# Kernel optimization log

Measured on AMD Instinct MI355X. Metric: run time of the kernel, lower is better.

The kernel has to match this reference:

```python
import jax, jax.numpy as jnp
import numpy as np

B, S, D, H = 2, 2048, 2048, 16
DH = D // H
EPS = 1e-5


def layernorm(x, gamma, beta):
    mu = jnp.mean(x, axis=-1, keepdims=True)
    var = jnp.var(x, axis=-1, keepdims=True)
    return (x - mu) * jax.lax.rsqrt(var + EPS) * gamma + beta


def setup_inputs() -> dict:
    key = jax.random.key(0)
    ks = jax.random.split(key, 10)
    sc = 1.0 / np.sqrt(D)
    return {
        "x": jax.random.normal(ks[0], (B, S, D), dtype=jnp.float32),
        "wq": jax.random.normal(ks[1], (D, D), dtype=jnp.float32) * sc,
        "bq": jnp.zeros((D,), jnp.float32),
        "wk": jax.random.normal(ks[2], (D, D), dtype=jnp.float32) * sc,
        "bk": jnp.zeros((D,), jnp.float32),
        "wv": jax.random.normal(ks[3], (D, D), dtype=jnp.float32) * sc,
        "bv": jnp.zeros((D,), jnp.float32),
        "wf": jax.random.normal(ks[4], (D, D), dtype=jnp.float32) * sc,
        "bf": jnp.zeros((D,), jnp.float32),
        "gamma": jnp.ones((D,), jnp.float32),
        "beta": jnp.zeros((D,), jnp.float32),
    }


def reference(x, wq, bq, wk, bk, wv, bv, wf, bf, gamma, beta):
    q = x @ wq + bq
    k = x @ wk + bk
    v = x @ wv + bv
    # split: [B,S,D] -> [B,H,S,DH]
    split = lambda t: t.reshape(B, S, H, DH).transpose(0, 2, 1, 3)
    q, k, v = split(q), split(k), split(v)
    s = jnp.einsum("bhqd,bhkd->bhqk", q, k) / np.sqrt(DH)
    p = jax.nn.softmax(s, axis=-1)
    o = jnp.einsum("bhqk,bhkd->bhqd", p, v)
    # faithful to original buggy concat: flat view of [B,H,S,DH] as [B,S,H*DH]
    o = o.reshape(B, S, H * DH)
    vb = o
    h1 = layernorm(o + x, gamma, beta)
    h2 = h1 @ wf + bf
    out = layernorm(h2 + vb, gamma, beta)
    return out
```

## Files before the change

### kernel.cpp

```cpp
#include <hip/hip_runtime.h>


#define B_ 2
#define S_ 2048
#define D_ 2048
#define H_ 16
#define DH_ 128

typedef __attribute__((ext_vector_type(8))) short s16x8;
typedef __attribute__((ext_vector_type(8))) unsigned short u16x8;
typedef __attribute__((ext_vector_type(4))) float f32x4;
typedef __attribute__((ext_vector_type(4))) unsigned short u16x4;

#define MFMA16(a, b, c) __builtin_amdgcn_mfma_f32_16x16x32_bf16(a, b, c, 0, 0, 0)

__device__ inline unsigned short f2bf(float f) {
  union { float f; unsigned u; } x; x.f = f;
  unsigned r = (x.u + 0x7fffu + ((x.u >> 16) & 1u)) >> 16;
  return (unsigned short)r;
}
__device__ inline float bf2f(unsigned short u) {
  union { unsigned u; float f; } x; x.u = ((unsigned)u) << 16;
  return x.f;
}
__device__ inline unsigned pack2bf(float a, float b) {
  unsigned ua = __builtin_bit_cast(unsigned, a) + 0x8000u;
  unsigned ub = __builtin_bit_cast(unsigned, b) + 0x8000u;
  return __builtin_amdgcn_perm(ub, ua, 0x07060302u);
}

__device__ inline void gld_lds16(const void* g, void* l) {
  __builtin_amdgcn_global_load_lds(
      (__attribute__((address_space(1))) void*)g,
      (__attribute__((address_space(3))) void*)l, 16, 0, 0);
}

__global__ __launch_bounds__(256) void prep_kernel(
    const float* __restrict__ x, unsigned short* __restrict__ xb,
    const float* __restrict__ w0, const float* __restrict__ w1,
    const float* __restrict__ w2, const float* __restrict__ w3,
    unsigned short* __restrict__ o0, unsigned short* __restrict__ o1,
    unsigned short* __restrict__ o2, unsigned short* __restrict__ o3) {
  int z = blockIdx.z;
  int t = threadIdx.x;
  if (z == 4) {
    int base = (blockIdx.y * 32 + blockIdx.x) * 16384 + t * 4;
#pragma unroll
    for (int p = 0; p < 16; ++p) {
      int i = base + p * 1024;
      float4 v = *(const float4*)&x[i];
      u16x4 o;
      o.x = f2bf(v.x); o.y = f2bf(v.y); o.z = f2bf(v.z); o.w = f2bf(v.w);
      *(u16x4*)&xb[i] = o;
    }
    return;
  }
  const float* W = z == 0 ? w0 : z == 1 ? w1 : z == 2 ? w2 : w3;
  unsigned short* WT = z == 0 ? o0 : z == 1 ? o1 : z == 2 ? o2 : o3;
  int n0 = blockIdx.x * 64, k0 = blockIdx.y * 128;
  int cl = t & 15, rw = t >> 4;
  int kb = k0 + rw * 8, nb = n0 + cl * 4;
  float4 f[8];
#pragma unroll
  for (int r = 0; r < 8; ++r) f[r] = *(const float4*)&W[(kb + r) * D_ + nb];
#define TPOSE(comp, i)                                                      \
  {                                                                         \
    u16x8 o = {f2bf(f[0].comp), f2bf(f[1].comp), f2bf(f[2].comp),           \
               f2bf(f[3].comp), f2bf(f[4].comp), f2bf(f[5].comp),           \
               f2bf(f[6].comp), f2bf(f[7].comp)};                           \
    *(u16x8*)&WT[(nb + i) * D_ + kb] = o;                                   \
  }
  TPOSE(x, 0) TPOSE(y, 1) TPOSE(z, 2) TPOSE(w, 3)
#undef TPOSE
}

__global__ __launch_bounds__(256) void gemm_qkv_kernel(
    const unsigned short* __restrict__ A, const unsigned short* __restrict__ W0,
    const unsigned short* __restrict__ W1, const unsigned short* __restrict__ W2,
    const float* __restrict__ b0, const float* __restrict__ b1,
    const float* __restrict__ b2, unsigned short* __restrict__ Qb,
    unsigned short* __restrict__ Kb, unsigned short* __restrict__ Vt,
    float qscale) {
  __shared__ short As[128 * 64];
  __shared__ short Bs[128 * 64];
  int wi = blockIdx.x >> 4;
  int n0 = (blockIdx.x & 15) * 128;
  const unsigned short* BT = wi == 0 ? W0 : wi == 1 ? W1 : W2;
  const float* bias = wi == 0 ? b0 : wi == 1 ? b1 : b2;
  float oscale = wi == 0 ? qscale : 1.0f;

  int t = threadIdx.x, lane = t & 63, w = t >> 6;
  int nl = lane & 15, q = lane >> 4;
  int m0 = blockIdx.y * 128;
  int wr = (w >> 1) * 64, wc = (w & 1) * 64;
  int swz = nl & 7;

  f32x4 acc[4][4];
  f32x4 z4 = {0.f, 0.f, 0.f, 0.f};
#pragma unroll
  for (int i = 0; i < 4; ++i)
#pragma unroll
    for (int j = 0; j < 4; ++j) acc[i][j] = z4;

  for (int kk = 0; kk < 2048; kk += 64) {
    __syncthreads();
#pragma unroll
    for (int i2 = 0; i2 < 4; ++i2) {
      int c = t + 256 * i2;
      int row = c >> 3, dc = (c & 7) ^ (row & 7);
      gld_lds16(&A[(m0 + row) * 2048 + kk + dc * 8], &As[c * 8]);
      gld_lds16(&BT[(n0 + row) * 2048 + kk + dc * 8], &Bs[c * 8]);
    }
    __syncthreads();
#pragma unroll
    for (int kc = 0; kc < 2; ++kc) {
      s16x8 af[4], bf[4];
#pragma unroll
      for (int i = 0; i < 4; ++i)
        af[i] = *(const s16x8*)&As[(wr + i * 16 + nl) * 64 +
                                   (((kc << 2) + q) ^ swz) * 8];
#pragma unroll
      for (int j = 0; j < 4; ++j)
        bf[j] = *(const s16x8*)&Bs[(wc + j * 16 + nl) * 64 +
                                   (((kc << 2) + q) ^ swz) * 8];
#pragma unroll
      for (int i = 0; i < 4; ++i)
#pragma unroll
        for (int j = 0; j < 4; ++j) acc[i][j] = MFMA16(af[i], bf[j], acc[i][j]);
    }
  }
#pragma unroll
  for (int i = 0; i < 4; ++i)
#pragma unroll
    for (int j = 0; j < 4; ++j) {
      int row = m0 + wr + i * 16 + q * 4;
      int col = n0 + wc + j * 16 + nl;
      float bv = bias[col];
      float v[4];
#pragma unroll
      for (int r = 0; r < 4; ++r) v[r] = (acc[i][j][r] + bv) * oscale;
      if (wi == 2) {
        unsigned d0 = pack2bf(v[0], v[1]), d1 = pack2bf(v[2], v[3]);
        long idx = ((long)(((row >> 11) * 16 + (col >> 7)) * 128 + (col & 127))) * 2048 +
                   (row & 2047);
        *(uint2*)&Vt[idx] = (uint2){d0, d1};
      } else {
        unsigned short* out = wi == 0 ? Qb : Kb;
#pragma unroll
        for (int r = 0; r < 4; ++r)
          out[(row + r) * 2048 + col] = f2bf(v[r]);
      }
    }
}

__global__ __launch_bounds__(256) void gemm_ff_kernel(
    const unsigned short* __restrict__ A, const unsigned short* __restrict__ BT,
    const float* __restrict__ bias, unsigned short* __restrict__ Cout) {
  __shared__ short As[128 * 64];
  __shared__ short Bs[128 * 64];
  int t = threadIdx.x, lane = t & 63, w = t >> 6;
  int nl = lane & 15, q = lane >> 4;
  int m0 = blockIdx.y * 128, n0 = blockIdx.x * 128;
  int wr = (w >> 1) * 64, wc = (w & 1) * 64;
  int swz = nl & 7;

  f32x4 acc[4][4];
  f32x4 z4 = {0.f, 0.f, 0.f, 0.f};
#pragma unroll
  for (int i = 0; i < 4; ++i)
#pragma unroll
    for (int j = 0; j < 4; ++j) acc[i][j] = z4;

  for (int kk = 0; kk < 2048; kk += 64) {
    __syncthreads();
#pragma unroll
    for (int i2 = 0; i2 < 4; ++i2) {
      int c = t + 256 * i2;
      int row = c >> 3, dc = (c & 7) ^ (row & 7);
      gld_lds16(&A[(m0 + row) * 2048 + kk + dc * 8], &As[c * 8]);
      gld_lds16(&BT[(n0 + row) * 2048 + kk + dc * 8], &Bs[c * 8]);
    }
    __syncthreads();
#pragma unroll
    for (int kc = 0; kc < 2; ++kc) {
      s16x8 af[4], bf[4];
#pragma unroll
      for (int i = 0; i < 4; ++i)
        af[i] = *(const s16x8*)&As[(wr + i * 16 + nl) * 64 +
                                   (((kc << 2) + q) ^ swz) * 8];
#pragma unroll
      for (int j = 0; j < 4; ++j)
        bf[j] = *(const s16x8*)&Bs[(wc + j * 16 + nl) * 64 +
                                   (((kc << 2) + q) ^ swz) * 8];
#pragma unroll
      for (int i = 0; i < 4; ++i)
#pragma unroll
        for (int j = 0; j < 4; ++j) acc[i][j] = MFMA16(af[i], bf[j], acc[i][j]);
    }
  }
#pragma unroll
  for (int i = 0; i < 4; ++i)
#pragma unroll
    for (int j = 0; j < 4; ++j) {
      int row = m0 + wr + i * 16 + q * 4;
      int col = n0 + wc + j * 16 + nl;
      float bv = bias[col];
#pragma unroll
      for (int r = 0; r < 4; ++r)
        Cout[(row + r) * 2048 + col] = f2bf(acc[i][j][r] + bv);
    }
}

__global__ __launch_bounds__(256, 2) void attn_kernel(
    const unsigned short* __restrict__ Q, const unsigned short* __restrict__ K,
    const unsigned short* __restrict__ VT, unsigned short* __restrict__ O) {
  __shared__ short KsA[8192], KsB[8192];
  __shared__ short VsA[8192], VsB[8192];
  __shared__ short Ps[8192];
  int t = threadIdx.x, lane = t & 63, w = t >> 6;
  int nl = lane & 15, q = lane >> 4;
  int i = blockIdx.x;
  int qb = i >> 5;
  int bh = (i & 7) + 8 * ((i >> 3) & 3);
  int b = bh >> 4, h = bh & 15;

  s16x8 qf[2][4];
  int qrow = b * S_ + qb * 128 + w * 32;
#pragma unroll
  for (int t2 = 0; t2 < 2; ++t2)
#pragma unroll
    for (int kc = 0; kc < 4; ++kc)
      qf[t2][kc] = *(const s16x8*)&Q[(qrow + t2 * 16 + nl) * D_ + h * DH_ + kc * 32 + q * 8];

  f32x4 z4 = {0.f, 0.f, 0.f, 0.f};
  f32x4 accO[2][8];
  f32x4 l4[2] = {z4, z4};
#pragma unroll
  for (int t2 = 0; t2 < 2; ++t2)
#pragma unroll
    for (int n8 = 0; n8 < 8; ++n8) accO[t2][n8] = z4;

  int swz = nl & 7;

  const unsigned short* kp[4];
  const unsigned short* vp[4];
#pragma unroll
  for (int i2 = 0; i2 < 4; ++i2) {
    int c = t + 256 * i2;
    int s = c >> 4, p = c & 15;
    kp[i2] = K + (long)(b * S_ + s) * D_ + h * DH_ + ((p ^ (s & 7)) * 8);
    int d = c >> 3, cp = c & 7, cs = cp ^ (d & 7);
    vp[i2] = VT + (long)(bh * DH_ + d) * S_ + cs * 8;
  }

#define STAGE(bufK, bufV)                           \
  {                                                 \
    _Pragma("unroll") for (int i2 = 0; i2 < 4; ++i2) { \
      gld_lds16(kp[i2], &bufK[(t + 256 * i2) * 8]); \
      gld_lds16(vp[i2], &bufV[(t + 256 * i2) * 8]); \
      kp[i2] += 64 * D_;                            \
      vp[i2] += 64;                                 \
    }                                               \
  }

  auto compute = [&](const short* Ks, const short* Vs) {
    f32x4 accS[2][4];
#pragma unroll
    for (int t2 = 0; t2 < 2; ++t2)
#pragma unroll
      for (int n = 0; n < 4; ++n) accS[t2][n] = z4;
    __builtin_amdgcn_s_setprio(1);
#pragma unroll
    for (int kc = 0; kc < 4; ++kc) {
      s16x8 kf[4];
#pragma unroll
      for (int n = 0; n < 4; ++n)
        kf[n] = *(const s16x8*)&Ks[(n * 16 + nl) * 128 +
                                   ((((kc << 2) + q) ^ swz)) * 8];
#pragma unroll
      for (int t2 = 0; t2 < 2; ++t2)
#pragma unroll
        for (int n = 0; n < 4; ++n)
          accS[t2][n] = MFMA16(kf[n], qf[t2][kc], accS[t2][n]);
    }
    __builtin_amdgcn_s_setprio(0);

#pragma unroll
    for (int t2 = 0; t2 < 2; ++t2) {
      int prow = (w * 32 + t2 * 16 + nl) * 64;
#pragma unroll
      for (int n = 0; n < 4; ++n) {
#pragma unroll
        for (int r = 0; r < 4; ++r)
          accS[t2][n][r] = __builtin_amdgcn_exp2f(accS[t2][n][r] - 16.0f);
        l4[t2] += accS[t2][n];
        unsigned d0 = pack2bf(accS[t2][n][0], accS[t2][n][1]);
        unsigned d1 = pack2bf(accS[t2][n][2], accS[t2][n][3]);
        int c8 = q + 4 * n;
        int off = prow + (((c8 >> 1) ^ swz) * 8 + (c8 & 1) * 4);
        *(uint2*)&Ps[off] = (uint2){d0, d1};
      }
    }

    __builtin_amdgcn_s_setprio(1);
#pragma unroll
    for (int ks = 0; ks < 2; ++ks) {
      s16x8 pf[2];
#pragma unroll
      for (int t2 = 0; t2 < 2; ++t2)
        pf[t2] = *(const s16x8*)&Ps[(w * 32 + t2 * 16 + nl) * 64 + ((4 * ks + q) ^ swz) * 8];
#pragma unroll
      for (int n8 = 0; n8 < 8; ++n8) {
        int d = n8 * 16 + nl;
        int cs = ks * 4 + q;
        int ci = d * 8 + (cs ^ (d & 7));
        s16x8 vf = *(const s16x8*)&Vs[ci * 8];
#pragma unroll
        for (int t2 = 0; t2 < 2; ++t2)
          accO[t2][n8] = MFMA16(vf, pf[t2], accO[t2][n8]);
      }
    }
    __builtin_amdgcn_s_setprio(0);
  };

  STAGE(KsA, VsA);
  for (int it = 0; it < 32; it += 2) {
    __syncthreads();
    STAGE(KsB, VsB);
    compute(KsA, VsA);
    __syncthreads();
    if (it + 2 < 32) STAGE(KsA, VsA);
    compute(KsB, VsB);
  }
#undef STAGE

#pragma unroll
  for (int t2 = 0; t2 < 2; ++t2) {
    float l = (l4[t2][0] + l4[t2][1]) + (l4[t2][2] + l4[t2][3]);
    l += __shfl_xor(l, 16);
    l += __shfl_xor(l, 32);
    float inv = 1.0f / l;
    int s = qb * 128 + w * 32 + t2 * 16 + nl;
    unsigned short* orow = &O[((long)(bh * S_ + s)) * DH_];
#pragma unroll
    for (int n8 = 0; n8 < 8; ++n8) {
      unsigned d0 = pack2bf(accO[t2][n8][0] * inv, accO[t2][n8][1] * inv);
      unsigned d1 = pack2bf(accO[t2][n8][2] * inv, accO[t2][n8][3] * inv);
      *(uint2*)&orow[n8 * 16 + q * 4] = (uint2){d0, d1};
    }
  }
}

template <int OUTBF, int INBF>
__global__ __launch_bounds__(256) void ln_kernel(
    const void* __restrict__ Ain, const unsigned short* __restrict__ Ob,
    const float* __restrict__ gamma, const float* __restrict__ beta,
    void* __restrict__ out) {
  int row = blockIdx.x, t = threadIdx.x;
  int lane = t & 63, w = t >> 6;
  int c0 = t * 8;
  float v[8], s = 0.f, s2 = 0.f;
  u16x8 ob = *(const u16x8*)&Ob[row * D_ + c0];
  if (INBF) {
    u16x8 a = *(const u16x8*)&((const unsigned short*)Ain)[row * D_ + c0];
#pragma unroll
    for (int p = 0; p < 8; ++p) v[p] = bf2f(a[p]);
  } else {
    float4 a0 = *(const float4*)&((const float*)Ain)[row * D_ + c0];
    float4 a1 = *(const float4*)&((const float*)Ain)[row * D_ + c0 + 4];
    v[0] = a0.x; v[1] = a0.y; v[2] = a0.z; v[3] = a0.w;
    v[4] = a1.x; v[5] = a1.y; v[6] = a1.z; v[7] = a1.w;
  }
#pragma unroll
  for (int p = 0; p < 8; ++p) {
    v[p] += bf2f(ob[p]);
    s += v[p]; s2 += v[p] * v[p];
  }
#pragma unroll
  for (int mk = 32; mk >= 1; mk >>= 1) {
    s += __shfl_xor(s, mk);
    s2 += __shfl_xor(s2, mk);
  }
  __shared__ float red[8];
  if (lane == 0) { red[w * 2] = s; red[w * 2 + 1] = s2; }
  __syncthreads();
  s = red[0] + red[2] + red[4] + red[6];
  s2 = red[1] + red[3] + red[5] + red[7];
  float mu = s * (1.0f / D_);
  float var = s2 * (1.0f / D_) - mu * mu;
  float rs = rsqrtf(var + 1e-5f);
  float4 g0 = *(const float4*)&gamma[c0], g1 = *(const float4*)&gamma[c0 + 4];
  float4 b0 = *(const float4*)&beta[c0], b1 = *(const float4*)&beta[c0 + 4];
  float g[8] = {g0.x, g0.y, g0.z, g0.w, g1.x, g1.y, g1.z, g1.w};
  float bb[8] = {b0.x, b0.y, b0.z, b0.w, b1.x, b1.y, b1.z, b1.w};
  float o[8];
#pragma unroll
  for (int p = 0; p < 8; ++p) o[p] = (v[p] - mu) * rs * g[p] + bb[p];
  if (OUTBF) {
    u16x8 ov;
#pragma unroll
    for (int p = 0; p < 8; ++p) ov[p] = f2bf(o[p]);
    *(u16x8*)&((unsigned short*)out)[row * D_ + c0] = ov;
  } else {
    float4 o0 = {o[0], o[1], o[2], o[3]}, o1 = {o[4], o[5], o[6], o[7]};
    *(float4*)&((float*)out)[row * D_ + c0] = o0;
    *(float4*)&((float*)out)[row * D_ + c0 + 4] = o1;
  }
}

extern "C" void kernel_launch(void* const* d_in, const int* in_sizes, int n_in,
                              void* d_out, int out_size, void* d_ws, size_t ws_size,
                              hipStream_t stream) {
  const float* x     = (const float*)d_in[0];
  const float* wq    = (const float*)d_in[1];
  const float* bq    = (const float*)d_in[2];
  const float* wk    = (const float*)d_in[3];
  const float* bk    = (const float*)d_in[4];
  const float* wv    = (const float*)d_in[5];
  const float* bv    = (const float*)d_in[6];
  const float* wf    = (const float*)d_in[7];
  const float* bfb   = (const float*)d_in[8];
  const float* gamma = (const float*)d_in[9];
  const float* beta  = (const float*)d_in[10];

  unsigned short* ws  = (unsigned short*)d_ws;
  unsigned short* WqT = ws;
  unsigned short* WkT = ws + 4194304;
  unsigned short* WvT = ws + 8388608;
  unsigned short* WfT = ws + 12582912;
  unsigned short* Xb  = ws + 16777216;
  unsigned short* Qb  = ws + 25165824;
  unsigned short* Kb  = ws + 33554432;
  unsigned short* Vt  = ws + 41943040;
  unsigned short* Ob  = Xb;
  unsigned short* H1  = Kb;
  unsigned short* H2b = Vt;

  const float scl2 = 0.08838834764831845f * 1.4426950408889634f;

  dim3 blk(256);
  prep_kernel<<<dim3(32, 16, 5), blk, 0, stream>>>(
      x, Xb, wq, wk, wv, wf, WqT, WkT, WvT, WfT);

  gemm_qkv_kernel<<<dim3(48, 32), blk, 0, stream>>>(
      Xb, WqT, WkT, WvT, bq, bk, bv, Qb, Kb, Vt, scl2);

  attn_kernel<<<dim3(512), blk, 0, stream>>>(Qb, Kb, Vt, Ob);

  ln_kernel<1, 0><<<dim3(4096), blk, 0, stream>>>(x, Ob, gamma, beta, (void*)H1);
  gemm_ff_kernel<<<dim3(16, 32), blk, 0, stream>>>(H1, WfT, bfb, H2b);
  ln_kernel<0, 1><<<dim3(4096), blk, 0, stream>>>(H2b, Ob, gamma, beta, d_out);
}
```

Measured before the change: 404.0 us.

## Replace GEMM kernels with 8-wave 256x128 triple-buffered pipelined GEMM

Merges the QKV and FF GEMMs into one templated kernel that uses 512 threads and a 256x128 output tile. A three-stage LDS ring prefetches K-tiles two iterations ahead, replacing the old load-then-sync-then-compute loop. The kernel also raises MFMA priority with s_setprio and remaps block IDs across XCDs, all to hide global-load latency and improve L2 locality. In exchange it uses far more LDS (144 KB) and allows only one block per CU, so latency hiding depends on the hand-written waitcnt schedule.

```diff
diff --git a/kernel.cpp b/kernel.cpp
--- a/kernel.cpp
+++ b/kernel.cpp
@@ -74,27 +74,54 @@
 #undef TPOSE
 }
 
-__global__ __launch_bounds__(256) void gemm_qkv_kernel(
+template <int QKV>
+__global__ __launch_bounds__(512, 1) void gemm8p_kernel(
     const unsigned short* __restrict__ A, const unsigned short* __restrict__ W0,
     const unsigned short* __restrict__ W1, const unsigned short* __restrict__ W2,
     const float* __restrict__ b0, const float* __restrict__ b1,
     const float* __restrict__ b2, unsigned short* __restrict__ Qb,
     unsigned short* __restrict__ Kb, unsigned short* __restrict__ Vt,
     float qscale) {
-  __shared__ short As[128 * 64];
-  __shared__ short Bs[128 * 64];
-  int wi = blockIdx.x >> 4;
-  int n0 = (blockIdx.x & 15) * 128;
-  const unsigned short* BT = wi == 0 ? W0 : wi == 1 ? W1 : W2;
-  const float* bias = wi == 0 ? b0 : wi == 1 ? b1 : b2;
-  float oscale = wi == 0 ? qscale : 1.0f;
+  __shared__ short As3[3][256 * 64];
+  __shared__ short Bs3[3][128 * 64];
+  int idx = blockIdx.x;
+  const int nwg = QKV ? 768 : 256;
+  const int cpx = nwg >> 3;
+  int wg = (idx & 7) * cpx + (idx >> 3);
+  int wi, mt, ntile;
+  if (QKV) {
+    wi = wg >> 8;
+    int rem = wg & 255;
+    mt = rem >> 4; ntile = rem & 15;
+  } else {
+    wi = 0; mt = wg >> 4; ntile = wg & 15;
+  }
+  int m0 = mt * 256, n0 = ntile * 128;
+  const unsigned short* BT = QKV ? (wi == 0 ? W0 : wi == 1 ? W1 : W2) : W0;
+  const float* bias = QKV ? (wi == 0 ? b0 : wi == 1 ? b1 : b2) : b0;
+  float oscale = (QKV && wi == 0) ? qscale : 1.0f;
 
   int t = threadIdx.x, lane = t & 63, w = t >> 6;
   int nl = lane & 15, q = lane >> 4;
-  int m0 = blockIdx.y * 128;
   int wr = (w >> 1) * 64, wc = (w & 1) * 64;
   int swz = nl & 7;
 
+  int aoff[4], boff[2], aldst[4], bldst[2];
+#pragma unroll
+  for (int l = 0; l < 4; ++l) {
+    int e = t + 512 * l;
+    int row = e >> 3, c = e & 7;
+    aoff[l] = (m0 + row) * 2048 + (c ^ (row & 7)) * 8;
+    aldst[l] = e * 8;
+  }
+#pragma unroll
+  for (int l = 0; l < 2; ++l) {
+    int e = t + 512 * l;
+    int row = e >> 3, c = e & 7;
+    boff[l] = (n0 + row) * 2048 + (c ^ (row & 7)) * 8;
+    bldst[l] = e * 8;
+  }
+
   f32x4 acc[4][4];
   f32x4 z4 = {0.f, 0.f, 0.f, 0.f};
 #pragma unroll
@@ -102,33 +129,72 @@
 #pragma unroll
     for (int j = 0; j < 4; ++j) acc[i][j] = z4;
 
-  for (int kk = 0; kk < 2048; kk += 64) {
-    __syncthreads();
-#pragma unroll
-    for (int i2 = 0; i2 < 4; ++i2) {
-      int c = t + 256 * i2;
-      int row = c >> 3, dc = (c & 7) ^ (row & 7);
-      gld_lds16(&A[(m0 + row) * 2048 + kk + dc * 8], &As[c * 8]);
-      gld_lds16(&BT[(n0 + row) * 2048 + kk + dc * 8], &Bs[c * 8]);
-    }
-    __syncthreads();
-#pragma unroll
-    for (int kc = 0; kc < 2; ++kc) {
-      s16x8 af[4], bf[4];
-#pragma unroll
-      for (int i = 0; i < 4; ++i)
-        af[i] = *(const s16x8*)&As[(wr + i * 16 + nl) * 64 +
-                                   (((kc << 2) + q) ^ swz) * 8];
-#pragma unroll
-      for (int j = 0; j < 4; ++j)
-        bf[j] = *(const s16x8*)&Bs[(wc + j * 16 + nl) * 64 +
-                                   (((kc << 2) + q) ^ swz) * 8];
-#pragma unroll
-      for (int i = 0; i < 4; ++i)
-#pragma unroll
-        for (int j = 0; j < 4; ++j) acc[i][j] = MFMA16(af[i], bf[j], acc[i][j]);
-    }
-  }
+#pragma unroll
+  for (int kt = 0; kt < 2; ++kt) {
+#pragma unroll
+    for (int l = 0; l < 4; ++l)
+      gld_lds16(&A[aoff[l] + kt * 64], &As3[kt][aldst[l]]);
+#pragma unroll
+    for (int l = 0; l < 2; ++l)
+      gld_lds16(&BT[boff[l] + kt * 64], &Bs3[kt][bldst[l]]);
+  }
+  asm volatile("s_waitcnt vmcnt(6)" ::: "memory");
+  __builtin_amdgcn_s_barrier();
+
+  int scur = 0;
+  for (int kt = 0; kt < 32; ++kt) {
+    const short* Asl = As3[scur];
+    const short* Bsl = Bs3[scur];
+    int sn = scur + 2; if (sn >= 3) sn -= 3;
+    short* Ad = As3[sn];
+    short* Bd = Bs3[sn];
+    int kst = (kt + 2) * 64;
+    bool st = kt < 30;
+    s16x8 af[4], bf[4];
+#pragma unroll
+    for (int i = 0; i < 4; ++i)
+      af[i] = *(const s16x8*)&Asl[(wr + i * 16 + nl) * 64 + (q ^ swz) * 8];
+#pragma unroll
+    for (int j = 0; j < 4; ++j)
+      bf[j] = *(const s16x8*)&Bsl[(wc + j * 16 + nl) * 64 + (q ^ swz) * 8];
+    if (st) {
+      gld_lds16(&A[aoff[0] + kst], &Ad[aldst[0]]);
+      gld_lds16(&A[aoff[1] + kst], &Ad[aldst[1]]);
+      gld_lds16(&BT[boff[0] + kst], &Bd[bldst[0]]);
+    }
+    __builtin_amdgcn_s_setprio(1);
+#pragma unroll
+    for (int i = 0; i < 4; ++i)
+#pragma unroll
+      for (int j = 0; j < 4; ++j) acc[i][j] = MFMA16(af[i], bf[j], acc[i][j]);
+    __builtin_amdgcn_s_setprio(0);
+#pragma unroll
+    for (int i = 0; i < 4; ++i)
+      af[i] = *(const s16x8*)&Asl[(wr + i * 16 + nl) * 64 + ((4 + q) ^ swz) * 8];
+#pragma unroll
+    for (int j = 0; j < 4; ++j)
+      bf[j] = *(const s16x8*)&Bsl[(wc + j * 16 + nl) * 64 + ((4 + q) ^ swz) * 8];
+    if (st) {
+      gld_lds16(&A[aoff[2] + kst], &Ad[aldst[2]]);
+      gld_lds16(&A[aoff[3] + kst], &Ad[aldst[3]]);
+      gld_lds16(&BT[boff[1] + kst], &Bd[bldst[1]]);
+    }
+    __builtin_amdgcn_s_setprio(1);
+#pragma unroll
+    for (int i = 0; i < 4; ++i)
+#pragma unroll
+      for (int j = 0; j < 4; ++j) acc[i][j] = MFMA16(af[i], bf[j], acc[i][j]);
+    __builtin_amdgcn_s_setprio(0);
+    if (kt < 31) {
+      if (st)
+        asm volatile("s_waitcnt vmcnt(6)" ::: "memory");
+      else
+        asm volatile("s_waitcnt vmcnt(0)" ::: "memory");
+      __builtin_amdgcn_s_barrier();
+    }
+    scur = scur + 1; if (scur == 3) scur = 0;
+  }
+
 #pragma unroll
   for (int i = 0; i < 4; ++i)
 #pragma unroll
@@ -139,75 +205,17 @@
       float v[4];
 #pragma unroll
       for (int r = 0; r < 4; ++r) v[r] = (acc[i][j][r] + bv) * oscale;
-      if (wi == 2) {
+      if (QKV && wi == 2) {
         unsigned d0 = pack2bf(v[0], v[1]), d1 = pack2bf(v[2], v[3]);
-        long idx = ((long)(((row >> 11) * 16 + (col >> 7)) * 128 + (col & 127))) * 2048 +
-                   (row & 2047);
-        *(uint2*)&Vt[idx] = (uint2){d0, d1};
+        long idxv = ((long)(((row >> 11) * 16 + (col >> 7)) * 128 + (col & 127))) * 2048 +
+                    (row & 2047);
+        *(uint2*)&Vt[idxv] = (uint2){d0, d1};
       } else {
-        unsigned short* out = wi == 0 ? Qb : Kb;
+        unsigned short* out = (QKV && wi == 1) ? Kb : Qb;
 #pragma unroll
         for (int r = 0; r < 4; ++r)
           out[(row + r) * 2048 + col] = f2bf(v[r]);
       }
-    }
-}
-
-__global__ __launch_bounds__(256) void gemm_ff_kernel(
-    const unsigned short* __restrict__ A, const unsigned short* __restrict__ BT,
-    const float* __restrict__ bias, unsigned short* __restrict__ Cout) {
-  __shared__ short As[128 * 64];
-  __shared__ short Bs[128 * 64];
-  int t = threadIdx.x, lane = t & 63, w = t >> 6;
-  int nl = lane & 15, q = lane >> 4;
-  int m0 = blockIdx.y * 128, n0 = blockIdx.x * 128;
-  int wr = (w >> 1) * 64, wc = (w & 1) * 64;
-  int swz = nl & 7;
-
-  f32x4 acc[4][4];
-  f32x4 z4 = {0.f, 0.f, 0.f, 0.f};
-#pragma unroll
-  for (int i = 0; i < 4; ++i)
-#pragma unroll
-    for (int j = 0; j < 4; ++j) acc[i][j] = z4;
-
-  for (int kk = 0; kk < 2048; kk += 64) {
-    __syncthreads();
-#pragma unroll
-    for (int i2 = 0; i2 < 4; ++i2) {
-      int c = t + 256 * i2;
-      int row = c >> 3, dc = (c & 7) ^ (row & 7);
-      gld_lds16(&A[(m0 + row) * 2048 + kk + dc * 8], &As[c * 8]);
-      gld_lds16(&BT[(n0 + row) * 2048 + kk + dc * 8], &Bs[c * 8]);
-    }
-    __syncthreads();
-#pragma unroll
-    for (int kc = 0; kc < 2; ++kc) {
-      s16x8 af[4], bf[4];
-#pragma unroll
-      for (int i = 0; i < 4; ++i)
-        af[i] = *(const s16x8*)&As[(wr + i * 16 + nl) * 64 +
-                                   (((kc << 2) + q) ^ swz) * 8];
-#pragma unroll
-      for (int j = 0; j < 4; ++j)
-        bf[j] = *(const s16x8*)&Bs[(wc + j * 16 + nl) * 64 +
-                                   (((kc << 2) + q) ^ swz) * 8];
-#pragma unroll
-      for (int i = 0; i < 4; ++i)
-#pragma unroll
-        for (int j = 0; j < 4; ++j) acc[i][j] = MFMA16(af[i], bf[j], acc[i][j]);
-    }
-  }
-#pragma unroll
-  for (int i = 0; i < 4; ++i)
-#pragma unroll
-    for (int j = 0; j < 4; ++j) {
-      int row = m0 + wr + i * 16 + q * 4;
-      int col = n0 + wc + j * 16 + nl;
-      float bv = bias[col];
-#pragma unroll
-      for (int r = 0; r < 4; ++r)
-        Cout[(row + r) * 2048 + col] = f2bf(acc[i][j][r] + bv);
     }
 }
 
@@ -442,12 +450,13 @@
   prep_kernel<<<dim3(32, 16, 5), blk, 0, stream>>>(
       x, Xb, wq, wk, wv, wf, WqT, WkT, WvT, WfT);
 
-  gemm_qkv_kernel<<<dim3(48, 32), blk, 0, stream>>>(
+  gemm8p_kernel<1><<<dim3(768), dim3(512), 0, stream>>>(
       Xb, WqT, WkT, WvT, bq, bk, bv, Qb, Kb, Vt, scl2);
 
   attn_kernel<<<dim3(512), blk, 0, stream>>>(Qb, Kb, Vt, Ob);
 
   ln_kernel<1, 0><<<dim3(4096), blk, 0, stream>>>(x, Ob, gamma, beta, (void*)H1);
-  gemm_ff_kernel<<<dim3(16, 32), blk, 0, stream>>>(H1, WfT, bfb, H2b);
+  gemm8p_kernel<0><<<dim3(256), dim3(512), 0, stream>>>(
+      H1, WfT, WfT, WfT, bfb, bfb, bfb, H2b, H2b, H2b, 1.0f);
   ln_kernel<0, 1><<<dim3(4096), blk, 0, stream>>>(H2b, Ob, gamma, beta, d_out);
 }
```

New measurement: 394.4 us. 2.4% less time.
